# Optimization experiments

Measured on AMD Instinct MI355X. Metric: run time of the kernel, lower is better.

Reference implementation:

```python
import jax, jax.numpy as jnp
import numpy as np

KERNEL_SIZE = 11
SIGMA = 1.5
K1 = 0.01
K2 = 0.03
DATA_RANGE = 1.0


def _gaussian_kernel_2d(kernel_size=KERNEL_SIZE, sigma=SIGMA):
    x = jnp.arange(kernel_size, dtype=jnp.float32) - kernel_size // 2
    k1d = jnp.exp(-0.5 * (x / sigma) ** 2)
    k1d = k1d / k1d.sum()
    k2d = k1d[None, :] * k1d[:, None]
    # OIHW layout, single in/out channel
    return k2d[None, None, :, :]


def _gauss_filter(x, kernel):
    pad = KERNEL_SIZE // 2
    return jax.lax.conv_general_dilated(
        x, kernel,
        window_strides=(1, 1),
        padding=[(pad, pad), (pad, pad)],
        dimension_numbers=('NCHW', 'OIHW', 'NCHW'))


def setup_inputs() -> dict:
    key = jax.random.key(0)
    k1, k2 = jax.random.split(key)
    B, C, H, W = 128, 1, 320, 320
    pred = jax.random.uniform(k1, (B, C, H, W), dtype=jnp.float32)
    target = jax.random.uniform(k2, (B, C, H, W), dtype=jnp.float32)
    return {"pred": pred, "target": target}


def reference(pred, target):
    kernel = _gaussian_kernel_2d()
    mu_x = _gauss_filter(pred, kernel)
    mu_y = _gauss_filter(target, kernel)
    mu_x_sq = mu_x * mu_x
    mu_y_sq = mu_y * mu_y
    mu_xy = mu_x * mu_y
    sigma_x_sq = _gauss_filter(pred * pred, kernel) - mu_x_sq
    sigma_y_sq = _gauss_filter(target * target, kernel) - mu_y_sq
    sigma_xy = _gauss_filter(pred * target, kernel) - mu_xy
    dr = jnp.asarray(DATA_RANGE, dtype=pred.dtype)
    c1 = (K1 * dr) ** 2
    c2 = (K2 * dr) ** 2
    numerator = (2 * mu_xy + c1) * (2 * sigma_xy + c2)
    denominator = (mu_x_sq + mu_y_sq + c1) * (sigma_x_sq + sigma_y_sq + c2)
    ssim_map = numerator / denominator
    return 1.0 - ssim_map.mean()
```

## Files before the change

### kernel.cpp

```cpp
#include <hip/hip_runtime.h>


namespace {
constexpr int W = 320, H = 320, B = 128;
constexpr int TH = 10;
constexpr int NSTRIPE = H / TH;
constexpr int NWAVE = B * NSTRIPE;
constexpr int ITERS = TH / 2;
constexpr float C1 = 1.0e-4f;
constexpr float C2 = 9.0e-4f;
constexpr int NSLOT = 128;
constexpr int SSTR = 16;
}

typedef _Float16 h2 __attribute__((ext_vector_type(2)));

__device__ __forceinline__ float fdot2f(h2 a, h2 b, float c) {
#if __has_builtin(__builtin_amdgcn_fdot2)
  return __builtin_amdgcn_fdot2(a, b, c, false);
#else
  return fmaf((float)a.x, (float)b.x, fmaf((float)a.y, (float)b.y, c));
#endif
}

__device__ __forceinline__ float rcpf(float x) {
  float r;
  asm("v_rcp_f32 %0, %1" : "=v"(r) : "v"(x));
  return r;
}

__device__ __forceinline__ h2 pack2(float a, float b) {
  return h2{(_Float16)a, (_Float16)b};
}

__device__ __forceinline__ h2 pkrtz(float a, float b) {
#if __has_builtin(__builtin_amdgcn_cvt_pkrtz)
  return __builtin_bit_cast(h2, __builtin_amdgcn_cvt_pkrtz(a, b));
#else
  return pack2(a, b);
#endif
}

__device__ __forceinline__ h2 dpp_up1(h2 v) {
  int r = __builtin_amdgcn_update_dpp(0, __builtin_bit_cast(int, v),
                                      0x138, 0xF, 0xF, true);
  return __builtin_bit_cast(h2, r);
}
__device__ __forceinline__ h2 dpp_dn1(h2 v) {
  int r = __builtin_amdgcn_update_dpp(0, __builtin_bit_cast(int, v),
                                      0x130, 0xF, 0xF, true);
  return __builtin_bit_cast(h2, r);
}

#define LOADP_RAW(ROW, A0, B0, A1, B1)                                        \
  do {                                                                        \
    const int r0_ = (ROW);                                                    \
    if (r0_ >= 0 && r0_ < H) {                                                \
      const float* p_ = P + r0_ * W;                                          \
      const float* t_ = T + r0_ * W;                                          \
      _Pragma("unroll") for (int c_ = 0; c_ < 5; ++c_) {                      \
        A0[c_] = p_[c_]; B0[c_] = t_[c_];                                     \
      }                                                                       \
    } else {                                                                  \
      _Pragma("unroll") for (int c_ = 0; c_ < 5; ++c_) {                      \
        A0[c_] = 0.f; B0[c_] = 0.f;                                           \
      }                                                                       \
    }                                                                         \
    if (r0_ + 1 >= 0 && r0_ + 1 < H) {                                        \
      const float* p_ = P + (r0_ + 1) * W;                                    \
      const float* t_ = T + (r0_ + 1) * W;                                    \
      _Pragma("unroll") for (int c_ = 0; c_ < 5; ++c_) {                      \
        A1[c_] = p_[c_]; B1[c_] = t_[c_];                                     \
      }                                                                       \
    } else {                                                                  \
      _Pragma("unroll") for (int c_ = 0; c_ < 5; ++c_) {                      \
        A1[c_] = 0.f; B1[c_] = 0.f;                                           \
      }                                                                       \
    }                                                                         \
  } while (0)

#define PACKTO(J, A0, B0, A1, B1)                                             \
  do {                                                                        \
    _Pragma("unroll") for (int c_ = 0; c_ < 5; ++c_) {                        \
      rp[J][c_] = pkrtz(A0[c_], A1[c_]);                                      \
      rt[J][c_] = pkrtz(B0[c_], B1[c_]);                                      \
    }                                                                         \
  } while (0)

#define HALO(PKc, L, R)                                                       \
  do {                                                                        \
    _Pragma("unroll") for (int c_ = 0; c_ < 5; ++c_) {                        \
      L[c_] = dpp_up1(PKc[c_]);                                               \
      R[c_] = dpp_dn1(PKc[c_]);                                               \
    }                                                                         \
  } while (0)

#define HBLUR(PKc, L, R, O)                                                   \
  do {                                                                        \
    _Pragma("unroll") for (int c_ = 0; c_ < 5; ++c_) {                        \
      h2 s1_ = WH[0] * ((c_ + 0 < 5) ? L[c_] : PKc[c_ - 5]);                  \
      _Pragma("unroll") for (int k_ = 1; k_ < 5; ++k_) {                      \
        const int i_ = c_ + k_;                                               \
        s1_ = WH[k_] * ((i_ < 5) ? L[i_] : PKc[i_ - 5]) + s1_;                \
      }                                                                       \
      h2 s2_ = WH[10] * R[c_];                                                \
      _Pragma("unroll") for (int k_ = 9; k_ >= 5; --k_) {                     \
        const int i_ = c_ + k_;                                               \
        s2_ = WH[k_] * ((i_ < 10) ? PKc[i_ - 5] : R[i_ - 10]) + s2_;          \
      }                                                                       \
      O[c_] = s1_ + s2_;                                                      \
    }                                                                         \
  } while (0)

__global__ __launch_bounds__(64) void ssim_main(
    const float* __restrict__ pred, const float* __restrict__ targ,
    float* __restrict__ sink, int slotmask, int sstr) {
  const int lane = threadIdx.x & 63;
  const int stripe = blockIdx.x;
  const int img = stripe / NSTRIPE;
  const int y0  = (stripe % NSTRIPE) * TH;

  const float* __restrict__ P = pred + (size_t)img * (W * H) + 5 * lane;
  const float* __restrict__ T = targ + (size_t)img * (W * H) + 5 * lane;

  constexpr float WF[11] = {0.00102838f, 0.00759885f, 0.03600081f, 0.10936069f,
                            0.21300553f, 0.26601171f, 0.21300553f, 0.10936069f,
                            0.03600081f, 0.00759885f, 0.00102838f};
  const h2 wAv[6] = {pack2(WF[0], WF[1]),  pack2(WF[2], WF[3]),
                     pack2(WF[4], WF[5]),  pack2(WF[6], WF[7]),
                     pack2(WF[8], WF[9]),  pack2(WF[10], 0.f)};
  const h2 wBv[6] = {pack2(0.f, WF[0]),    pack2(WF[1], WF[2]),
                     pack2(WF[3], WF[4]),  pack2(WF[5], WF[6]),
                     pack2(WF[7], WF[8]),  pack2(WF[9], WF[10])};
  h2 WH[11];
#pragma unroll
  for (int k = 0; k < 11; ++k) WH[k] = pack2(WF[k], WF[k]);

  h2 rp[6][5], rt[6][5];
  float nfA[5], ntA[5], nfB[5], ntB[5];

  {
    float aA[5], bA[5], cA[5], dA[5];
    float aB[5], bB[5], cB[5], dB[5];
    LOADP_RAW(y0 - 5, aA, bA, cA, dA);
    LOADP_RAW(y0 - 3, aB, bB, cB, dB);
    PACKTO(1, aA, bA, cA, dA);
    LOADP_RAW(y0 - 1, aA, bA, cA, dA);
    PACKTO(2, aB, bB, cB, dB);
    LOADP_RAW(y0 + 1, aB, bB, cB, dB);
    PACKTO(3, aA, bA, cA, dA);
    LOADP_RAW(y0 + 3, aA, bA, cA, dA);
    PACKTO(4, aB, bB, cB, dB);
    LOADP_RAW(y0 + 5, nfA, ntA, nfB, ntB);
    PACKTO(5, aA, bA, cA, dA);
  }

  float acc = 0.f;

#pragma unroll 1
  for (int it = 0; it < ITERS; ++it) {
#pragma unroll
    for (int j = 0; j < 5; ++j)
#pragma unroll
      for (int c = 0; c < 5; ++c) {
        rp[j][c] = rp[j + 1][c];
        rt[j][c] = rt[j + 1][c];
      }
    PACKTO(5, nfA, ntA, nfB, ntB);
    if (it + 1 < ITERS) LOADP_RAW(y0 + 2 * it + 7, nfA, ntA, nfB, ntB);

    h2 PK[5][5];
#pragma unroll
    for (int c = 0; c < 5; ++c) {
      float mpA = 0, mtA = 0, ppA = 0, ttA = 0, ptA = 0;
      float mpB = 0, mtB = 0, ppB = 0, ttB = 0, ptB = 0;
#pragma unroll
      for (int j = 0; j < 6; ++j) {
        const h2 a = rp[j][c], b = rt[j][c];
        const h2 aa = a * a, bb = b * b, ab = a * b;
        const h2 wa = wAv[j], wb = wBv[j];
        mpA = fdot2f(wa, a, mpA);
        mtA = fdot2f(wa, b, mtA);
        ppA = fdot2f(wa, aa, ppA);
        ttA = fdot2f(wa, bb, ttA);
        ptA = fdot2f(wa, ab, ptA);
        mpB = fdot2f(wb, a, mpB);
        mtB = fdot2f(wb, b, mtB);
        ppB = fdot2f(wb, aa, ppB);
        ttB = fdot2f(wb, bb, ttB);
        ptB = fdot2f(wb, ab, ptB);
      }
      PK[0][c] = pkrtz(mpA, mpB);
      PK[1][c] = pkrtz(mtA, mtB);
      PK[2][c] = pkrtz(ppA, ppB);
      PK[3][c] = pkrtz(ttA, ttB);
      PK[4][c] = pkrtz(ptA, ptB);
    }

    h2 OUT[5][5];
#pragma unroll
    for (int ch = 0; ch < 5; ++ch) {
      h2 L[5], R[5];
      HALO(PK[ch], L, R);
      HBLUR(PK[ch], L, R, OUT[ch]);
    }

#pragma unroll
    for (int c = 0; c < 5; ++c) {
#pragma unroll
      for (int r = 0; r < 2; ++r) {
        const float mx = r ? (float)OUT[0][c].y : (float)OUT[0][c].x;
        const float my = r ? (float)OUT[1][c].y : (float)OUT[1][c].x;
        const float xx = r ? (float)OUT[2][c].y : (float)OUT[2][c].x;
        const float yy = r ? (float)OUT[3][c].y : (float)OUT[3][c].x;
        const float xy = r ? (float)OUT[4][c].y : (float)OUT[4][c].x;
        const float mxx = mx * mx, myy = my * my, mxy = mx * my;
        const float vx = xx - mxx, vy = yy - myy, vxy = xy - mxy;
        const float num = (2.f * mxy + C1) * (2.f * vxy + C2);
        const float den = (mxx + myy + C1) * (vx + vy + C2);
        acc = fmaf(num, rcpf(den), acc);
      }
    }
  }

#pragma unroll
  for (int off = 32; off; off >>= 1) acc += __shfl_xor(acc, off, 64);
  if (lane == 0) atomicAdd(sink + (stripe & slotmask) * sstr, acc);
}

__global__ void ssim_final(const float* __restrict__ sink, int nslot, int sstr,
                           float* __restrict__ out) {
  const int tid = threadIdx.x;
  float v = 0.f;
  for (int s = tid; s < nslot; s += 64) v += sink[s * sstr];
#pragma unroll
  for (int off = 32; off; off >>= 1) v += __shfl_xor(v, off, 64);
  if (tid == 0) out[0] = 1.f - v / 13107200.f;
}

extern "C" void kernel_launch(void* const* d_in, const int* in_sizes, int n_in,
                              void* d_out, int out_size, void* d_ws, size_t ws_size,
                              hipStream_t stream) {
  (void)in_sizes; (void)n_in; (void)out_size;
  const float* pred = (const float*)d_in[0];
  const float* targ = (const float*)d_in[1];
  float* out = (float*)d_out;

  float* sink;
  int nslot, sstr;
  const size_t need = (size_t)NSLOT * SSTR * sizeof(float);
  if (ws_size >= need) {
    sink = (float*)d_ws;
    nslot = NSLOT;
    sstr = SSTR;
  } else {
    sink = out;
    nslot = 1;
    sstr = 0;
  }
  (void)hipMemsetAsync(sink, 0, nslot == 1 ? sizeof(float) : need, stream);
  ssim_main<<<dim3(NWAVE), dim3(64), 0, stream>>>(pred, targ, sink, nslot - 1, sstr);
  ssim_final<<<1, 64, 0, stream>>>(sink, nslot, sstr, out);
}
```

Baseline: 60.46 us.

## Filter sum/difference channels to cut Gaussian-blurred statistics from five to four

Inputs are transformed into half-sum and half-difference channels, s=(p+t)/2 and d=(p-t)/2. Blurring s, d, s² and d² is enough to rebuild mu_x, mu_y and the variance and covariance terms through a sum/difference identity. This removes one of five vertical and horizontal blur channels, along with its DPP halo exchange and packed products. The cost is an extra packed fp16 add, subtract and scale per input, and the fp16 subtraction of squared terms may change rounding.

Result: faster. 57.14 us (-5.5%).

```diff
diff --git a/kernel.cpp b/kernel.cpp
--- a/kernel.cpp
+++ b/kernel.cpp
@@ -82,8 +82,10 @@
 #define PACKTO(J, A0, B0, A1, B1)                                             \
   do {                                                                        \
     _Pragma("unroll") for (int c_ = 0; c_ < 5; ++c_) {                        \
-      rp[J][c_] = pkrtz(A0[c_], A1[c_]);                                      \
-      rt[J][c_] = pkrtz(B0[c_], B1[c_]);                                      \
+      const h2 hp_ = pkrtz(A0[c_], A1[c_]);                                   \
+      const h2 ht_ = pkrtz(B0[c_], B1[c_]);                                   \
+      rs[J][c_] = (hp_ + ht_) * H05;                                          \
+      rd[J][c_] = (hp_ - ht_) * H05;                                          \
     }                                                                         \
   } while (0)
 
@@ -135,8 +137,9 @@
   h2 WH[11];
 #pragma unroll
   for (int k = 0; k < 11; ++k) WH[k] = pack2(WF[k], WF[k]);
-
-  h2 rp[6][5], rt[6][5];
+  const h2 H05 = pack2(0.5f, 0.5f);
+
+  h2 rs[6][5], rd[6][5];
   float nfA[5], ntA[5], nfB[5], ntB[5];
 
   {
@@ -163,43 +166,40 @@
     for (int j = 0; j < 5; ++j)
 #pragma unroll
       for (int c = 0; c < 5; ++c) {
-        rp[j][c] = rp[j + 1][c];
-        rt[j][c] = rt[j + 1][c];
+        rs[j][c] = rs[j + 1][c];
+        rd[j][c] = rd[j + 1][c];
       }
     PACKTO(5, nfA, ntA, nfB, ntB);
     if (it + 1 < ITERS) LOADP_RAW(y0 + 2 * it + 7, nfA, ntA, nfB, ntB);
 
-    h2 PK[5][5];
+    h2 PK[4][5];
 #pragma unroll
     for (int c = 0; c < 5; ++c) {
-      float mpA = 0, mtA = 0, ppA = 0, ttA = 0, ptA = 0;
-      float mpB = 0, mtB = 0, ppB = 0, ttB = 0, ptB = 0;
+      float sA = 0, dA = 0, ssA = 0, ddA = 0;
+      float sB = 0, dB = 0, ssB = 0, ddB = 0;
 #pragma unroll
       for (int j = 0; j < 6; ++j) {
-        const h2 a = rp[j][c], b = rt[j][c];
-        const h2 aa = a * a, bb = b * b, ab = a * b;
+        const h2 a = rs[j][c], b = rd[j][c];
+        const h2 aa = a * a, bb = b * b;
         const h2 wa = wAv[j], wb = wBv[j];
-        mpA = fdot2f(wa, a, mpA);
-        mtA = fdot2f(wa, b, mtA);
-        ppA = fdot2f(wa, aa, ppA);
-        ttA = fdot2f(wa, bb, ttA);
-        ptA = fdot2f(wa, ab, ptA);
-        mpB = fdot2f(wb, a, mpB);
-        mtB = fdot2f(wb, b, mtB);
-        ppB = fdot2f(wb, aa, ppB);
-        ttB = fdot2f(wb, bb, ttB);
-        ptB = fdot2f(wb, ab, ptB);
+        sA  = fdot2f(wa, a, sA);
+        dA  = fdot2f(wa, b, dA);
+        ssA = fdot2f(wa, aa, ssA);
+        ddA = fdot2f(wa, bb, ddA);
+        sB  = fdot2f(wb, a, sB);
+        dB  = fdot2f(wb, b, dB);
+        ssB = fdot2f(wb, aa, ssB);
+        ddB = fdot2f(wb, bb, ddB);
       }
-      PK[0][c] = pkrtz(mpA, mpB);
-      PK[1][c] = pkrtz(mtA, mtB);
-      PK[2][c] = pkrtz(ppA, ppB);
-      PK[3][c] = pkrtz(ttA, ttB);
-      PK[4][c] = pkrtz(ptA, ptB);
+      PK[0][c] = pkrtz(sA, sB);
+      PK[1][c] = pkrtz(dA, dB);
+      PK[2][c] = pkrtz(ssA, ssB);
+      PK[3][c] = pkrtz(ddA, ddB);
     }
 
-    h2 OUT[5][5];
-#pragma unroll
-    for (int ch = 0; ch < 5; ++ch) {
+    h2 OUT[4][5];
+#pragma unroll
+    for (int ch = 0; ch < 4; ++ch) {
       h2 L[5], R[5];
       HALO(PK[ch], L, R);
       HBLUR(PK[ch], L, R, OUT[ch]);
@@ -209,16 +209,18 @@
     for (int c = 0; c < 5; ++c) {
 #pragma unroll
       for (int r = 0; r < 2; ++r) {
-        const float mx = r ? (float)OUT[0][c].y : (float)OUT[0][c].x;
-        const float my = r ? (float)OUT[1][c].y : (float)OUT[1][c].x;
-        const float xx = r ? (float)OUT[2][c].y : (float)OUT[2][c].x;
-        const float yy = r ? (float)OUT[3][c].y : (float)OUT[3][c].x;
-        const float xy = r ? (float)OUT[4][c].y : (float)OUT[4][c].x;
-        const float mxx = mx * mx, myy = my * my, mxy = mx * my;
-        const float vx = xx - mxx, vy = yy - myy, vxy = xy - mxy;
-        const float num = (2.f * mxy + C1) * (2.f * vxy + C2);
-        const float den = (mxx + myy + C1) * (vx + vy + C2);
-        acc = fmaf(num, rcpf(den), acc);
+        const float u = r ? (float)OUT[0][c].y : (float)OUT[0][c].x;
+        const float v = r ? (float)OUT[1][c].y : (float)OUT[1][c].x;
+        const float w = r ? (float)OUT[2][c].y : (float)OUT[2][c].x;
+        const float x = r ? (float)OUT[3][c].y : (float)OUT[3][c].x;
+        const float uu = u * u, vv = v * v;
+        const float A  = uu + vv;
+        const float Bq = uu - vv;
+        const float num1 = fmaf(2.f, Bq, C1);
+        const float num2 = fmaf(2.f, (w - x) - Bq, C2);
+        const float den1 = fmaf(2.f, A, C1);
+        const float den2 = fmaf(2.f, (w + x) - A, C2);
+        acc = fmaf(num1 * num2, rcpf(den1 * den2), acc);
       }
     }
   }
```
